# Optimization experiments

Hardware: AMD Instinct MI355X
Metric: run time of the kernel (lower is better)

The kernel has to match this reference:

```python
import jax, jax.numpy as jnp
import numpy as np

N_NODES = 100000
N_EDGES = 3200000
D_FEAT = 64


def setup_inputs() -> dict:
    key = jax.random.key(0)
    k1, k2, k3 = jax.random.split(key, 3)
    inputs = jax.random.normal(k1, (N_NODES, D_FEAT), dtype=jnp.float32)
    rows = jax.random.randint(k2, (N_EDGES,), 0, N_NODES, dtype=jnp.int32)
    cols = jax.random.randint(k3, (N_EDGES,), 0, N_NODES, dtype=jnp.int32)
    return {"inputs": inputs, "rows": rows, "cols": cols}


def reference(inputs, rows, cols):
    # adj is a binary sparse [N, N] matrix given as COO edges (rows[e], cols[e]) -> 1.0
    n = inputs.shape[0]
    # degrees = adj.sum(dim=1): count of outgoing edges per row
    deg = jax.ops.segment_sum(jnp.ones_like(rows, dtype=inputs.dtype), rows,
                              num_segments=n)  # [N]
    # degrees + (degrees == 0): avoid div-by-zero for isolated nodes
    deg = deg + (deg == 0).astype(inputs.dtype)
    # spmm(adj, inputs): sum neighbor features into each row
    agg = jax.ops.segment_sum(inputs[cols], rows, num_segments=n)  # [N, d]
    return agg / deg[:, None]
```

## Files before the change

kernel.cpp:

```cpp
#include <hip/hip_runtime.h>
#include <hip/hip_fp16.h>

#define D_FEAT 64
#define TILE_EDGES 12500
#define SC_THREADS 512
#define ROWS_PER_BUK 128
#define BUK_SHIFT 7
#define STRIDE 4480
#define K_STASH ((TILE_EDGES + SC_THREADS * 4 - 1) / (SC_THREADS * 4))
#define G_STASH ((STRIDE + 511) / 512)

__global__ void __launch_bounds__(SC_THREADS) scatter_kernel(
    const float* __restrict__ x, __half* __restrict__ x16,
    const int* __restrict__ rows, const int* __restrict__ cols,
    int* __restrict__ gcount, int* __restrict__ ebuf,
    int n_edges, int nbuk, int n4)
{
    __shared__ int lh[1024];
    __shared__ int lscan[1024];
    __shared__ int lgb[1024];
    __shared__ int lsort[TILE_EDGES];
    __shared__ int wsum[8];

    const int t = threadIdx.x;
    const int w = t >> 6;
    const int lane = t & 63;

    {
        const int per = (n4 + gridDim.x - 1) / gridDim.x;
        const int s0 = blockIdx.x * per;
        const int e0 = min(s0 + per, n4);
        for (int i = s0 + t; i < e0; i += SC_THREADS) {
            float4 v = ((const float4*)x)[i];
            ushort4 u;
            u.x = __half_as_ushort(__float2half(v.x));
            u.y = __half_as_ushort(__float2half(v.y));
            u.z = __half_as_ushort(__float2half(v.z));
            u.w = __half_as_ushort(__float2half(v.w));
            ((ushort4*)x16)[i] = u;
        }
    }

    lh[t] = 0; lh[t + 512] = 0;
    __syncthreads();

    const int tb = blockIdx.x * TILE_EDGES;
    const int te = min(tb + TILE_EDGES, n_edges);

    int4 r4s[K_STASH], c4s[K_STASH];
    #pragma unroll
    for (int k = 0; k < K_STASH; ++k) {
        const int e = tb + t * 4 + k * (SC_THREADS * 4);
        if (e + 4 <= te) {
            int4 r4 = *(const int4*)&rows[e];
            int4 c4 = *(const int4*)&cols[e];
            r4s[k] = r4; c4s[k] = c4;
            atomicAdd(&lh[r4.x >> BUK_SHIFT], 1);
            atomicAdd(&lh[r4.y >> BUK_SHIFT], 1);
            atomicAdd(&lh[r4.z >> BUK_SHIFT], 1);
            atomicAdd(&lh[r4.w >> BUK_SHIFT], 1);
        } else {
            r4s[k] = make_int4(-1, -1, -1, -1);
            c4s[k] = make_int4(0, 0, 0, 0);
            for (int q = e; q < te; ++q) atomicAdd(&lh[rows[q] >> BUK_SHIFT], 1);
        }
    }
    __syncthreads();

    const int c0 = lh[2 * t], c1 = lh[2 * t + 1];
    const int s2 = c0 + c1;
    {
        int val = s2;
        #pragma unroll
        for (int ofs = 1; ofs < 64; ofs <<= 1) {
            int n = __shfl_up(val, ofs, 64);
            if (lane >= ofs) val += n;
        }
        if (lane == 63) wsum[w] = val;
        __syncthreads();
        int off = 0;
        #pragma unroll
        for (int k = 0; k < 8; ++k) off += (k < w) ? wsum[k] : 0;
        const int excl = off + val - s2;
        lscan[2 * t] = excl;
        lscan[2 * t + 1] = excl + c0;
        lgb[2 * t]     = c0 ? atomicAdd(&gcount[2 * t], c0) : 0;
        lgb[2 * t + 1] = c1 ? atomicAdd(&gcount[2 * t + 1], c1) : 0;
        lh[2 * t] = excl;
        lh[2 * t + 1] = excl + c0;
    }
    __syncthreads();

    #pragma unroll
    for (int k = 0; k < K_STASH; ++k) {
        int4 r4 = r4s[k];
        int4 c4 = c4s[k];
        if (r4.x >= 0) {
            int p0 = atomicAdd(&lh[r4.x >> BUK_SHIFT], 1);
            int p1 = atomicAdd(&lh[r4.y >> BUK_SHIFT], 1);
            int p2 = atomicAdd(&lh[r4.z >> BUK_SHIFT], 1);
            int p3 = atomicAdd(&lh[r4.w >> BUK_SHIFT], 1);
            lsort[p0] = ((r4.x & (ROWS_PER_BUK - 1)) << 17) | c4.x;
            lsort[p1] = ((r4.y & (ROWS_PER_BUK - 1)) << 17) | c4.y;
            lsort[p2] = ((r4.z & (ROWS_PER_BUK - 1)) << 17) | c4.z;
            lsort[p3] = ((r4.w & (ROWS_PER_BUK - 1)) << 17) | c4.w;
        } else {
            const int e = tb + t * 4 + k * (SC_THREADS * 4);
            for (int q = e; q < te; ++q) {
                int r = rows[q], c = cols[q];
                int pos = atomicAdd(&lh[r >> BUK_SHIFT], 1);
                lsort[pos] = ((r & (ROWS_PER_BUK - 1)) << 17) | c;
            }
        }
    }
    __syncthreads();

    const int qw = t >> 4;
    const int ql = t & 15;
    for (int b = qw; b < nbuk; b += 32) {
        const int ls = lscan[b];
        const int cnt = lh[b] - ls;
        const int gb = lgb[b];
        for (int i = ql; i < cnt; i += 16) {
            int gpos = gb + i;
            if (gpos < STRIDE) ebuf[b * STRIDE + gpos] = lsort[ls + i];
        }
    }
}

__global__ void __launch_bounds__(512) gather_kernel(
    const uint4* __restrict__ x4, const int* __restrict__ gcount,
    const int* __restrict__ ebuf, float* __restrict__ out, int n_nodes)
{
    __shared__ int lcol[STRIDE];
    __shared__ int lh[ROWS_PER_BUK];
    __shared__ int lscan[ROWS_PER_BUK];
    __shared__ int lcur[ROWS_PER_BUK];
    const int b = blockIdx.x;
    const int t = threadIdx.x;

    const int start = b * STRIDE;
    int cnt = gcount[b];
    if (cnt > STRIDE) cnt = STRIDE;

    if (t < ROWS_PER_BUK) lh[t] = 0;
    __syncthreads();

    int pst[G_STASH];
    #pragma unroll
    for (int k = 0; k < G_STASH; ++k) {
        const int i = t + k * 512;
        pst[k] = (i < cnt) ? ebuf[start + i] : -1;
        if (pst[k] >= 0) atomicAdd(&lh[pst[k] >> 17], 1);
    }
    __syncthreads();

    if (t < 64) {
        int cA = lh[2 * t], cB = lh[2 * t + 1];
        int s2 = cA + cB;
        int val = s2;
        #pragma unroll
        for (int ofs = 1; ofs < 64; ofs <<= 1) {
            int n = __shfl_up(val, ofs, 64);
            if (t >= ofs) val += n;
        }
        int excl = val - s2;
        lscan[2 * t] = excl;
        lscan[2 * t + 1] = excl + cA;
        lcur[2 * t] = excl;
        lcur[2 * t + 1] = excl + cA;
    }
    __syncthreads();

    #pragma unroll
    for (int k = 0; k < G_STASH; ++k) {
        if (pst[k] >= 0) {
            int pos = atomicAdd(&lcur[pst[k] >> 17], 1);
            lcol[pos] = pst[k] & 0x1FFFF;
        }
    }
    __syncthreads();

    const int w = t >> 6;
    const int lane = t & 63;
    const int eg = lane >> 3;
    const int g2 = lane & 7;

    union U { uint4 u; __half2 h2[4]; };

    for (int rr = 0; rr < 16; ++rr) {
        const int r = w * 16 + rr;
        const int row = (b << BUK_SHIFT) + r;
        const int s = lscan[r];
        const int d = lh[r];
        const int e = s + d;

        const __half2 z = __float2half2_rn(0.0f);
        __half2 h[4];
        #pragma unroll
        for (int k = 0; k < 4; ++k) h[k] = z;

        int j = s;
        for (; j + 32 <= e; j += 32) {
            int cA = lcol[j + eg], cB = lcol[j + 8 + eg];
            int cC = lcol[j + 16 + eg], cD = lcol[j + 24 + eg];
            U A, B, C, D;
            A.u = x4[cA * 8 + g2];
            B.u = x4[cB * 8 + g2];
            C.u = x4[cC * 8 + g2];
            D.u = x4[cD * 8 + g2];
            #pragma unroll
            for (int k = 0; k < 4; ++k)
                h[k] = __hadd2(h[k], __hadd2(__hadd2(A.h2[k], B.h2[k]),
                                             __hadd2(C.h2[k], D.h2[k])));
        }
        for (; j + 16 <= e; j += 16) {
            int cA = lcol[j + eg], cB = lcol[j + 8 + eg];
            U A, B;
            A.u = x4[cA * 8 + g2];
            B.u = x4[cB * 8 + g2];
            #pragma unroll
            for (int k = 0; k < 4; ++k)
                h[k] = __hadd2(h[k], __hadd2(A.h2[k], B.h2[k]));
        }
        for (; j + 8 <= e; j += 8) {
            int c = lcol[j + eg];
            U A;
            A.u = x4[c * 8 + g2];
            #pragma unroll
            for (int k = 0; k < 4; ++k) h[k] = __hadd2(h[k], A.h2[k]);
        }
        int rem = e - j;
        if (eg < rem) {
            int c = lcol[j + eg];
            U A;
            A.u = x4[c * 8 + g2];
            #pragma unroll
            for (int k = 0; k < 4; ++k) h[k] = __hadd2(h[k], A.h2[k]);
        }

        float a[8];
        #pragma unroll
        for (int k = 0; k < 4; ++k) {
            float2 f = __half22float2(h[k]);
            a[2 * k] = f.x;
            a[2 * k + 1] = f.y;
        }
        #pragma unroll
        for (int k = 0; k < 8; ++k) {
            a[k] += __shfl_down(a[k], 8, 64);
            a[k] += __shfl_down(a[k], 16, 64);
            a[k] += __shfl_down(a[k], 32, 64);
        }

        if (eg == 0 && row < n_nodes) {
            const float inv = 1.0f / (float)(d > 0 ? d : 1);
            float4* o = (float4*)(out + ((long)row << 6) + (g2 << 3));
            o[0] = make_float4(a[0] * inv, a[1] * inv, a[2] * inv, a[3] * inv);
            o[1] = make_float4(a[4] * inv, a[5] * inv, a[6] * inv, a[7] * inv);
        }
    }
}

extern "C" void kernel_launch(void* const* d_in, const int* in_sizes, int n_in,
                              void* d_out, int out_size, void* d_ws, size_t ws_size,
                              hipStream_t stream) {
    const float* x  = (const float*)d_in[0];
    const int* rows = (const int*)d_in[1];
    const int* cols = (const int*)d_in[2];
    float* out = (float*)d_out;

    const int n_nodes = in_sizes[0] / D_FEAT;
    const int n_edges = in_sizes[1];
    const int n_feat_total = in_sizes[0];
    const int n4 = n_feat_total / 4;

    const int nbuk   = (n_nodes + ROWS_PER_BUK - 1) >> BUK_SHIFT;
    const int ntiles = (n_edges + TILE_EDGES - 1) / TILE_EDGES;

    __half* x16 = (__half*)d_ws;
    int* gcount = (int*)(x16 + n_feat_total);
    int* ebuf   = gcount + nbuk;

    hipMemsetAsync(gcount, 0, (size_t)nbuk * sizeof(int), stream);

    scatter_kernel<<<ntiles, SC_THREADS, 0, stream>>>(
        x, x16, rows, cols, gcount, ebuf, n_edges, nbuk, n4);

    gather_kernel<<<nbuk, 512, 0, stream>>>((const uint4*)x16, gcount, ebuf, out, n_nodes);
}
```

Before: 170.4 us.

## Split gather into column-range phases with per-row register accumulators

Each row's edge list in the gather kernel is now sorted into four sub-bins by column range (col>>15), using a 512-bin shared histogram and a block-wide scan. The 16 rows per wave then accumulate across four phases, one per column quarter, with a barrier between phases. The goal is that all blocks read roughly the same quarter of the feature table at the same time, improving L2 hit rate for the random row gathers. The cost is 64 half2 accumulators held per thread, which raises register pressure and may cut occupancy, plus extra barriers and less unrolled loads per row.

```diff
diff --git a/kernel.cpp b/kernel.cpp
--- a/kernel.cpp
+++ b/kernel.cpp
@@ -9,6 +9,8 @@
 #define STRIDE 4480
 #define K_STASH ((TILE_EDGES + SC_THREADS * 4 - 1) / (SC_THREADS * 4))
 #define G_STASH ((STRIDE + 511) / 512)
+#define NPH 4
+#define NBIN (ROWS_PER_BUK * NPH)
 
 __global__ void __launch_bounds__(SC_THREADS) scatter_kernel(
     const float* __restrict__ x, __half* __restrict__ x16,
@@ -133,17 +135,21 @@
     const int* __restrict__ ebuf, float* __restrict__ out, int n_nodes)
 {
     __shared__ int lcol[STRIDE];
-    __shared__ int lh[ROWS_PER_BUK];
-    __shared__ int lscan[ROWS_PER_BUK];
-    __shared__ int lcur[ROWS_PER_BUK];
+    __shared__ int lh2[NBIN];
+    __shared__ int lsc[NBIN];
+    __shared__ int lcur[NBIN];
+    __shared__ int wsum[8];
+
     const int b = blockIdx.x;
     const int t = threadIdx.x;
+    const int w = t >> 6;
+    const int lane = t & 63;
 
     const int start = b * STRIDE;
     int cnt = gcount[b];
     if (cnt > STRIDE) cnt = STRIDE;
 
-    if (t < ROWS_PER_BUK) lh[t] = 0;
+    lh2[t] = 0;
     __syncthreads();
 
     int pst[G_STASH];
@@ -151,98 +157,95 @@
     for (int k = 0; k < G_STASH; ++k) {
         const int i = t + k * 512;
         pst[k] = (i < cnt) ? ebuf[start + i] : -1;
-        if (pst[k] >= 0) atomicAdd(&lh[pst[k] >> 17], 1);
-    }
-    __syncthreads();
-
-    if (t < 64) {
-        int cA = lh[2 * t], cB = lh[2 * t + 1];
-        int s2 = cA + cB;
-        int val = s2;
+        if (pst[k] >= 0) {
+            int c = pst[k] & 0x1FFFF;
+            atomicAdd(&lh2[((pst[k] >> 17) << 2) | (c >> 15)], 1);
+        }
+    }
+    __syncthreads();
+
+    {
+        int c = lh2[t];
+        int val = c;
         #pragma unroll
         for (int ofs = 1; ofs < 64; ofs <<= 1) {
             int n = __shfl_up(val, ofs, 64);
-            if (t >= ofs) val += n;
-        }
-        int excl = val - s2;
-        lscan[2 * t] = excl;
-        lscan[2 * t + 1] = excl + cA;
-        lcur[2 * t] = excl;
-        lcur[2 * t + 1] = excl + cA;
+            if (lane >= ofs) val += n;
+        }
+        if (lane == 63) wsum[w] = val;
+        __syncthreads();
+        int off = 0;
+        #pragma unroll
+        for (int k = 0; k < 8; ++k) off += (k < w) ? wsum[k] : 0;
+        int excl = val + off - c;
+        lsc[t] = excl;
+        lcur[t] = excl;
     }
     __syncthreads();
 
     #pragma unroll
     for (int k = 0; k < G_STASH; ++k) {
         if (pst[k] >= 0) {
-            int pos = atomicAdd(&lcur[pst[k] >> 17], 1);
-            lcol[pos] = pst[k] & 0x1FFFF;
-        }
-    }
-    __syncthreads();
-
-    const int w = t >> 6;
-    const int lane = t & 63;
+            int c = pst[k] & 0x1FFFF;
+            int bin = ((pst[k] >> 17) << 2) | (c >> 15);
+            int pos = atomicAdd(&lcur[bin], 1);
+            if (pos < STRIDE) lcol[pos] = c;
+        }
+    }
+    __syncthreads();
+
     const int eg = lane >> 3;
     const int g2 = lane & 7;
 
     union U { uint4 u; __half2 h2[4]; };
-
+    const uint4 uz = make_uint4(0u, 0u, 0u, 0u);
+    const __half2 z = __float2half2_rn(0.0f);
+
+    __half2 h[16][4];
+    #pragma unroll
+    for (int rr = 0; rr < 16; ++rr)
+        #pragma unroll
+        for (int k = 0; k < 4; ++k) h[rr][k] = z;
+
+    for (int p = 0; p < NPH; ++p) {
+        #pragma unroll
+        for (int rr = 0; rr < 16; ++rr) {
+            const int r = w * 16 + rr;
+            const int bin = (r << 2) | p;
+            const int s = lsc[bin];
+            const int n = lh2[bin];
+
+            U A, B;
+            A.u = uz; B.u = uz;
+            if (eg < n)     A.u = x4[lcol[s + eg] * 8 + g2];
+            if (eg + 8 < n) B.u = x4[lcol[s + 8 + eg] * 8 + g2];
+            #pragma unroll
+            for (int k = 0; k < 4; ++k)
+                h[rr][k] = __hadd2(h[rr][k], __hadd2(A.h2[k], B.h2[k]));
+
+            const int e = s + n;
+            for (int j = s + 16; j < e; j += 8) {
+                if (eg < e - j) {
+                    U C;
+                    C.u = x4[lcol[j + eg] * 8 + g2];
+                    #pragma unroll
+                    for (int k = 0; k < 4; ++k) h[rr][k] = __hadd2(h[rr][k], C.h2[k]);
+                }
+            }
+        }
+        __syncthreads();
+    }
+
+    #pragma unroll
     for (int rr = 0; rr < 16; ++rr) {
         const int r = w * 16 + rr;
         const int row = (b << BUK_SHIFT) + r;
-        const int s = lscan[r];
-        const int d = lh[r];
-        const int e = s + d;
-
-        const __half2 z = __float2half2_rn(0.0f);
-        __half2 h[4];
-        #pragma unroll
-        for (int k = 0; k < 4; ++k) h[k] = z;
-
-        int j = s;
-        for (; j + 32 <= e; j += 32) {
-            int cA = lcol[j + eg], cB = lcol[j + 8 + eg];
-            int cC = lcol[j + 16 + eg], cD = lcol[j + 24 + eg];
-            U A, B, C, D;
-            A.u = x4[cA * 8 + g2];
-            B.u = x4[cB * 8 + g2];
-            C.u = x4[cC * 8 + g2];
-            D.u = x4[cD * 8 + g2];
-            #pragma unroll
-            for (int k = 0; k < 4; ++k)
-                h[k] = __hadd2(h[k], __hadd2(__hadd2(A.h2[k], B.h2[k]),
-                                             __hadd2(C.h2[k], D.h2[k])));
-        }
-        for (; j + 16 <= e; j += 16) {
-            int cA = lcol[j + eg], cB = lcol[j + 8 + eg];
-            U A, B;
-            A.u = x4[cA * 8 + g2];
-            B.u = x4[cB * 8 + g2];
-            #pragma unroll
-            for (int k = 0; k < 4; ++k)
-                h[k] = __hadd2(h[k], __hadd2(A.h2[k], B.h2[k]));
-        }
-        for (; j + 8 <= e; j += 8) {
-            int c = lcol[j + eg];
-            U A;
-            A.u = x4[c * 8 + g2];
-            #pragma unroll
-            for (int k = 0; k < 4; ++k) h[k] = __hadd2(h[k], A.h2[k]);
-        }
-        int rem = e - j;
-        if (eg < rem) {
-            int c = lcol[j + eg];
-            U A;
-            A.u = x4[c * 8 + g2];
-            #pragma unroll
-            for (int k = 0; k < 4; ++k) h[k] = __hadd2(h[k], A.h2[k]);
-        }
+        const int d = (lsc[(r << 2) | 3] + lh2[(r << 2) | 3]) - lsc[r << 2];
 
         float a[8];
         #pragma unroll
         for (int k = 0; k < 4; ++k) {
-            float2 f = __half22float2(h[k]);
+            float2 f = __half22float2(h[rr][k]);
             a[2 * k] = f.x;
             a[2 * k + 1] = f.y;
         }
```

Result: slower. 211.6 us (+24.2%).
